# Performance work log

Measured on AMD Instinct MI355X. Metric: run time of the kernel, lower is better.

The kernel has to match this reference:

```python
import jax, jax.numpy as jnp
import numpy as np

B, L, D, H = 2, 2048, 768, 12
HD = D // H  # 64
BASE = 10000


def rope_tables(seq_len, head_dim, base):
    # inverse frequencies over even indices, angles [L, hd/2] -> duplicated to [L, hd]
    inv_freq = 1.0 / (base ** (jnp.arange(0, head_dim, 2, dtype=jnp.float32) / head_dim))
    angles = jnp.arange(seq_len, dtype=jnp.float32)[:, None] * inv_freq[None, :]
    cos = jnp.concatenate([jnp.cos(angles), jnp.cos(angles)], axis=-1)  # [L, hd]
    sin = jnp.concatenate([jnp.sin(angles), jnp.sin(angles)], axis=-1)
    return cos, sin


def rotate_half(x):
    x1, x2 = jnp.split(x, 2, axis=-1)
    return jnp.concatenate([-x2, x1], axis=-1)


def setup_inputs() -> dict:
    key = jax.random.key(0)
    k0, k1, k2 = jax.random.split(key, 3)
    s = 0.02
    return {
        "input_embeddings": jax.random.normal(k0, (B, L, D), dtype=jnp.float32),
        "w_qkv": jax.random.normal(k1, (D, 3 * D), dtype=jnp.float32) * s,
        "b_qkv": jnp.zeros((3 * D,), dtype=jnp.float32),
        "w_out": jax.random.normal(k2, (D, D), dtype=jnp.float32) * s,
        "b_out": jnp.zeros((D,), dtype=jnp.float32),
    }


def reference(input_embeddings, w_qkv, b_qkv, w_out, b_out):
    # QKV projection and head split: b l (h d) -> b h l d
    qkv = input_embeddings @ w_qkv + b_qkv
    q, k, v = jnp.split(qkv, 3, axis=-1)
    to_heads = lambda t: t.reshape(B, L, H, HD).transpose(0, 2, 1, 3)
    q, k, v = map(to_heads, (q, k, v))

    # RoPE (start_pos=0, no kv cache)
    cos, sin = rope_tables(L, HD, BASE)  # [L, HD], broadcasts over b,h
    q = q * cos + rotate_half(q) * sin
    k = k * cos + rotate_half(k) * sin

    # NOTE: source divides by sqrt(d.size(3)) = sqrt(key_seq_len), not sqrt(head_dim)
    scores = jnp.einsum("bhqd,bhkd->bhqk", q, k) / jnp.sqrt(jnp.float32(L))

    causal_mask = jnp.triu(jnp.ones((L, L), dtype=bool), 1)
    neg_inf = -jnp.finfo(scores.dtype).max
    scores = jnp.where(causal_mask, neg_inf, scores)

    probs = jax.nn.softmax(scores, axis=-1)  # dropout disabled (eval)
    attn_out = jnp.einsum("bhqk,bhkd->bhqd", probs, v)
    attn_out = attn_out.transpose(0, 2, 1, 3).reshape(B, L, D)  # b h l d -> b l (h d)
    output = attn_out @ w_out + b_out
    return output, probs
```

## Files before the change

kernel.cpp:

```cpp
#include <hip/hip_runtime.h>
#include <math.h>

#define B_  2
#define L_  2048
#define D_  768
#define H_  12
#define HD_ 64
#define M_  (B_*L_)
#define N3_ (3*D_)
#define OUT_ELEMS ((size_t)B_*L_*D_)

static constexpr float kScale = 0.022097086912079608f;
static constexpr float kLog2_10000_div32 = 0.415241011860920f;

typedef __attribute__((ext_vector_type(8))) short short8;
typedef __attribute__((ext_vector_type(4))) float f32x4;

__device__ __forceinline__ unsigned short f2bf(float f) {
  union { float f; unsigned u; } v; v.f = f;
  unsigned r = v.u + 0x7FFFu + ((v.u >> 16) & 1u);
  return (unsigned short)(r >> 16);
}

__device__ __forceinline__ void async_cp16(const void* g, void* l) {
  __builtin_amdgcn_global_load_lds((const __attribute__((address_space(1))) void*)g,
                                   (__attribute__((address_space(3))) void*)l, 16, 0, 0);
}

__global__ __launch_bounds__(256) void bf16conv_kernel(const float* __restrict__ in,
                                                       unsigned short* __restrict__ out)
{
  const int idx = blockIdx.x * 256 + threadIdx.x;
  const float* src = in + (size_t)idx * 8;
  float4 a = *(const float4*)src;
  float4 b = *(const float4*)(src + 4);
  unsigned short t[8];
  t[0] = f2bf(a.x); t[1] = f2bf(a.y); t[2] = f2bf(a.z); t[3] = f2bf(a.w);
  t[4] = f2bf(b.x); t[5] = f2bf(b.y); t[6] = f2bf(b.z); t[7] = f2bf(b.w);
  *(uint4*)(out + (size_t)idx * 8) = *(uint4*)t;
}

__global__ __launch_bounds__(256) void wtrans_kernel(const float* __restrict__ in,
                                                     unsigned short* __restrict__ out,
                                                     int K, int N)
{
  __shared__ __align__(16) unsigned short T[64][72];
  const int n0 = blockIdx.x * 64;
  const int k0 = blockIdx.y * 64;
  const int tid = threadIdx.x;
  const int row = tid >> 2;
  const int col = (tid & 3) * 16;
  {
    const float* src = in + (size_t)(k0 + row) * N + n0 + col;
    unsigned short tmp[16];
#pragma unroll
    for (int j = 0; j < 16; j += 4) {
      float4 v = *(const float4*)(src + j);
      tmp[j] = f2bf(v.x); tmp[j + 1] = f2bf(v.y); tmp[j + 2] = f2bf(v.z); tmp[j + 3] = f2bf(v.w);
    }
    *(uint4*)&T[row][col]     = *(uint4*)tmp;
    *(uint4*)&T[row][col + 8] = *(uint4*)(tmp + 8);
  }
  __syncthreads();
  unsigned short tmp[16];
#pragma unroll
  for (int j = 0; j < 16; ++j) tmp[j] = T[col + j][row];
  unsigned short* dst = out + (size_t)(n0 + row) * K + k0 + col;
  *(uint4*)dst       = *(uint4*)tmp;
  *(uint4*)(dst + 8) = *(uint4*)(tmp + 8);
}

__global__ __launch_bounds__(256) void vtrans_kernel(const unsigned short* __restrict__ vb,
                                                     unsigned short* __restrict__ vt)
{
  __shared__ __align__(16) unsigned short T[64][72];
  const int bh = blockIdx.y;
  const int l0 = blockIdx.x * 64;
  const int tid = threadIdx.x;
  const int row = tid >> 2;
  const int col = (tid & 3) * 16;
  {
    const unsigned short* src = vb + ((size_t)bh * L_ + l0 + row) * HD_ + col;
    *(uint4*)&T[row][col]     = *(const uint4*)src;
    *(uint4*)&T[row][col + 8] = *(const uint4*)(src + 8);
  }
  __syncthreads();
  unsigned short tmp[16];
#pragma unroll
  for (int j = 0; j < 16; ++j) tmp[j] = T[col + j][row];
  unsigned short* dst = vt + ((size_t)bh * HD_ + row) * L_ + l0 + col;
  *(uint4*)dst       = *(uint4*)tmp;
  *(uint4*)(dst + 8) = *(uint4*)(tmp + 8);
}

__global__ __launch_bounds__(256) void gemm_mfma_kernel(
    const unsigned short* __restrict__ A, const unsigned short* __restrict__ Bt,
    const float* __restrict__ bias, float* __restrict__ C,
    int M, int N, int K, int mode,
    unsigned short* __restrict__ qp, unsigned short* __restrict__ kp,
    unsigned short* __restrict__ vp)
{
  __shared__ __align__(16) unsigned short As[128 * 32];
  __shared__ __align__(16) unsigned short Bs[128 * 32];

  const int tid  = threadIdx.x;
  const int w    = tid >> 6;
  const int lane = tid & 63;
  const int m16  = lane & 15;
  const int quad = lane >> 4;
  const int wr   = w & 1;
  const int wc   = w >> 1;

  const int bm = blockIdx.y * 128;
  const int bn = blockIdx.x * 128;

  const int s0 = w * 128 + lane;
  const int s1 = s0 + 64;
  const int r0 = s0 >> 2, c0 = (s0 & 3) ^ (r0 & 3);
  const int r1 = s1 >> 2, c1 = (s1 & 3) ^ (r1 & 3);
  const unsigned short* gA0 = A + (size_t)(bm + r0) * K + c0 * 8;
  const unsigned short* gA1 = A + (size_t)(bm + r1) * K + c1 * 8;
  const unsigned short* gB0 = Bt + (size_t)(bn + r0) * K + c0 * 8;
  const unsigned short* gB1 = Bt + (size_t)(bn + r1) * K + c1 * 8;
  unsigned short* lA0 = As + (w * 128) * 8;
  unsigned short* lA1 = As + (w * 128 + 64) * 8;
  unsigned short* lB0 = Bs + (w * 128) * 8;
  unsigned short* lB1 = Bs + (w * 128 + 64) * 8;

  const int sw = quad ^ (m16 & 3);
  const short8* pA[4];
  const short8* pB[4];
#pragma unroll
  for (int i = 0; i < 4; ++i) {
    const int ra = wr * 64 + i * 16 + m16;
    const int rb = wc * 64 + i * 16 + m16;
    pA[i] = (const short8*)(As + ra * 32 + sw * 8);
    pB[i] = (const short8*)(Bs + rb * 32 + sw * 8);
  }

  f32x4 acc[4][4];
#pragma unroll
  for (int i = 0; i < 4; ++i)
#pragma unroll
    for (int j = 0; j < 4; ++j) { acc[i][j][0] = 0.f; acc[i][j][1] = 0.f; acc[i][j][2] = 0.f; acc[i][j][3] = 0.f; }

  for (int k0 = 0; k0 < K; k0 += 32) {
    async_cp16(gA0 + k0, lA0);
    async_cp16(gA1 + k0, lA1);
    async_cp16(gB0 + k0, lB0);
    async_cp16(gB1 + k0, lB1);
    __syncthreads();
    short8 af[4], bfr[4];
#pragma unroll
    for (int i = 0; i < 4; ++i) { af[i] = *pA[i]; bfr[i] = *pB[i]; }
#pragma unroll
    for (int i = 0; i < 4; ++i)
#pragma unroll
      for (int j = 0; j < 4; ++j)
        acc[i][j] = __builtin_amdgcn_mfma_f32_16x16x32_bf16(af[i], bfr[j], acc[i][j], 0, 0, 0);
    __syncthreads();
  }

  if (mode == 0) {
#pragma unroll
    for (int j = 0; j < 4; ++j) {
      const int n = bn + wc * 64 + j * 16 + m16;
      const float bj = bias[n];
#pragma unroll
      for (int i = 0; i < 4; ++i) {
        const int mrow = bm + wr * 64 + i * 16 + quad * 4;
#pragma unroll
        for (int r2 = 0; r2 < 4; ++r2)
          C[(size_t)(mrow + r2) * N + n] = acc[i][j][r2] + bj;
      }
    }
  } else {
    const int segbase = bn + wc * 64;
    const int which = segbase / D_;
    const int h = (segbase - which * D_) >> 6;
    unsigned short* dstT = (which == 0) ? qp : (which == 1) ? kp : vp;
    float bj[4];
#pragma unroll
    for (int og = 0; og < 4; ++og) bj[og] = bias[segbase + og * 16 + m16];
    const float invfA = exp2f(-(float)m16 * kLog2_10000_div32);
    const float invfB = exp2f(-(float)(16 + m16) * kLog2_10000_div32);

#pragma unroll
    for (int i = 0; i < 4; ++i) {
      const int mrow = bm + wr * 64 + i * 16 + quad * 4;
#pragma unroll
      for (int r2 = 0; r2 < 4; ++r2) {
        const int m = mrow + r2;
        const int bi = m >> 11;
        const int li = m & (L_ - 1);
        float vals[4];
#pragma unroll
        for (int og = 0; og < 4; ++og) vals[og] = acc[i][og][r2] + bj[og];
        unsigned short* drow = dstT + (((size_t)(bi * H_ + h)) * L_ + li) * HD_;
        if (which == 2) {
#pragma unroll
          for (int og = 0; og < 4; ++og) drow[og * 16 + m16] = f2bf(vals[og]);
        } else {
          const float fl = (float)li;
#pragma unroll
          for (int og = 0; og < 4; ++og) {
            const int d = og * 16 + m16;
            const float theta = fl * ((og & 1) ? invfB : invfA);
            float sv, cv;
            __sincosf(theta, &sv, &cv);
            const float part = vals[og ^ 2];
            const float rot = (og < 2) ? -part : part;
            drow[d] = f2bf(vals[og] * cv + rot * sv);
          }
        }
      }
    }
  }
}

__global__ __launch_bounds__(256) void attn_mfma_kernel(
    const unsigned short* __restrict__ qb, const unsigned short* __restrict__ kb,
    const unsigned short* __restrict__ vt, float* __restrict__ probs,
    unsigned short* __restrict__ attnb)
{
  __shared__ __align__(16) unsigned short Ks[64][72];
  __shared__ __align__(16) unsigned short Vs[64][72];
  __shared__ __align__(16) unsigned short Pb[4][16][72];

  const int tid  = threadIdx.x;
  const int w    = tid >> 6;
  const int lane = tid & 63;
  const int m16  = lane & 15;
  const int quad = lane >> 4;

  const int bh = blockIdx.y;
  const int qt = (int)gridDim.x - 1 - (int)blockIdx.x;
  const int q0 = qt * 64;
  const int bb = bh / H_;
  const int hh = bh - bb * H_;
  const int ktiles = qt + 1;
  const int qrow_base = q0 + w * 16;

  const unsigned short* kbase = kb + (size_t)bh * L_ * HD_;
  const unsigned short* vbase = vt + (size_t)bh * HD_ * L_;

  const unsigned short* qp = qb + ((size_t)bh * L_ + qrow_base + m16) * HD_ + quad * 8;
  const short8 qf0 = *(const short8*)(qp);
  const short8 qf1 = *(const short8*)(qp + 32);

  const int srow = tid >> 2;
  const int scol = (tid & 3) * 16;

  float lsum[4] = {0.f, 0.f, 0.f, 0.f};
  for (int kt = 0; kt < ktiles; ++kt) {
    const int k0 = kt * 64;
    __syncthreads();
    {
      const unsigned short* src = kbase + (size_t)(k0 + srow) * HD_ + scol;
      *(uint4*)&Ks[srow][scol]     = *(const uint4*)src;
      *(uint4*)&Ks[srow][scol + 8] = *(const uint4*)(src + 8);
    }
    __syncthreads();
#pragma unroll
    for (int cg = 0; cg < 4; ++cg) {
      const short8 b0 = *(const short8*)&Ks[cg * 16 + m16][quad * 8];
      const short8 b1 = *(const short8*)&Ks[cg * 16 + m16][32 + quad * 8];
      f32x4 s = {0.f, 0.f, 0.f, 0.f};
      s = __builtin_amdgcn_mfma_f32_16x16x32_bf16(qf0, b0, s, 0, 0, 0);
      s = __builtin_amdgcn_mfma_f32_16x16x32_bf16(qf1, b1, s, 0, 0, 0);
      const int kcol = k0 + cg * 16 + m16;
#pragma unroll
      for (int r2 = 0; r2 < 4; ++r2) {
        const int qrow = qrow_base + quad * 4 + r2;
        const float e = __expf(s[r2] * kScale);
        lsum[r2] += (kcol <= qrow) ? e : 0.f;
      }
    }
  }
  float linv[4];
#pragma unroll
  for (int r2 = 0; r2 < 4; ++r2) {
    float v = lsum[r2];
    v += __shfl_xor(v, 1, 64);
    v += __shfl_xor(v, 2, 64);
    v += __shfl_xor(v, 4, 64);
    v += __shfl_xor(v, 8, 64);
    linv[r2] = 1.f / v;
  }

  f32x4 oacc[4];
#pragma unroll
  for (int og = 0; og < 4; ++og) { oacc[og][0]=0.f; oacc[og][1]=0.f; oacc[og][2]=0.f; oacc[og][3]=0.f; }

  for (int kt = 0; kt < ktiles; ++kt) {
    const int k0 = kt * 64;
    __syncthreads();
    {
      const unsigned short* srck = kbase + (size_t)(k0 + srow) * HD_ + scol;
      *(uint4*)&Ks[srow][scol]     = *(const uint4*)srck;
      *(uint4*)&Ks[srow][scol + 8] = *(const uint4*)(srck + 8);
      const unsigned short* srcv = vbase + (size_t)srow * L_ + k0 + scol;
      *(uint4*)&Vs[srow][scol]     = *(const uint4*)srcv;
      *(uint4*)&Vs[srow][scol + 8] = *(const uint4*)(srcv + 8);
    }
    __syncthreads();
#pragma unroll
    for (int cg = 0; cg < 4; ++cg) {
      const short8 b0 = *(const short8*)&Ks[cg * 16 + m16][quad * 8];
      const short8 b1 = *(const short8*)&Ks[cg * 16 + m16][32 + quad * 8];
      f32x4 s = {0.f, 0.f, 0.f, 0.f};
      s = __builtin_amdgcn_mfma_f32_16x16x32_bf16(qf0, b0, s, 0, 0, 0);
      s = __builtin_amdgcn_mfma_f32_16x16x32_bf16(qf1, b1, s, 0, 0, 0);
      const int kcol = k0 + cg * 16 + m16;
#pragma unroll
      for (int r2 = 0; r2 < 4; ++r2) {
        const int qrow = qrow_base + quad * 4 + r2;
        const float p = (kcol <= qrow) ? __expf(s[r2] * kScale) * linv[r2] : 0.f;
        probs[((size_t)bh * L_ + qrow) * L_ + kcol] = p;
        Pb[w][quad * 4 + r2][cg * 16 + m16] = f2bf(p);
      }
    }
    const short8 pa0 = *(const short8*)&Pb[w][m16][quad * 8];
    const short8 pa1 = *(const short8*)&Pb[w][m16][32 + quad * 8];
#pragma unroll
    for (int og = 0; og < 4; ++og) {
      const short8 v0 = *(const short8*)&Vs[og * 16 + m16][quad * 8];
      const short8 v1 = *(const short8*)&Vs[og * 16 + m16][32 + quad * 8];
      oacc[og] = __builtin_amdgcn_mfma_f32_16x16x32_bf16(pa0, v0, oacc[og], 0, 0, 0);
      oacc[og] = __builtin_amdgcn_mfma_f32_16x16x32_bf16(pa1, v1, oacc[og], 0, 0, 0);
    }
  }

  {
    const float4 z4 = make_float4(0.f, 0.f, 0.f, 0.f);
#pragma unroll
    for (int r2 = 0; r2 < 4; ++r2) {
      float* pr = probs + ((size_t)bh * L_ + qrow_base + quad * 4 + r2) * L_;
      for (int c0 = ktiles * 64; c0 < L_; c0 += 64)
        *(float4*)(pr + c0 + m16 * 4) = z4;
    }
  }

#pragma unroll
  for (int og = 0; og < 4; ++og)
#pragma unroll
    for (int r2 = 0; r2 < 4; ++r2)
      attnb[((size_t)bb * L_ + qrow_base + quad * 4 + r2) * D_ + hh * HD_ + og * 16 + m16] =
          f2bf(oacc[og][r2]);
}

extern "C" void kernel_launch(void* const* d_in, const int* in_sizes, int n_in,
                              void* d_out, int out_size, void* d_ws, size_t ws_size,
                              hipStream_t stream)
{
  const float* x     = (const float*)d_in[0];
  const float* w_qkv = (const float*)d_in[1];
  const float* b_qkv = (const float*)d_in[2];
  const float* w_out = (const float*)d_in[3];
  const float* b_out = (const float*)d_in[4];

  float* out   = (float*)d_out;
  float* probs = out + OUT_ELEMS;

  const size_t NE = (size_t)B_ * H_ * L_ * HD_;
  unsigned short* qbw   = (unsigned short*)d_ws;
  unsigned short* kbw   = qbw + NE;
  unsigned short* vbw   = kbw + NE;
  unsigned short* vtw   = vbw + NE;
  unsigned short* xbw   = vtw + NE;
  unsigned short* attnb = xbw + NE;
  unsigned short* wqT   = attnb + NE;
  unsigned short* woT   = wqT + (size_t)N3_ * D_;

  bf16conv_kernel<<<(int)(OUT_ELEMS / 8 / 256), 256, 0, stream>>>(x, xbw);
  wtrans_kernel<<<dim3(N3_ / 64, D_ / 64), 256, 0, stream>>>(w_qkv, wqT, D_, N3_);
  wtrans_kernel<<<dim3(D_ / 64, D_ / 64), 256, 0, stream>>>(w_out, woT, D_, D_);

  gemm_mfma_kernel<<<dim3(N3_ / 128, M_ / 128), 256, 0, stream>>>(
      xbw, wqT, b_qkv, nullptr, M_, N3_, D_, 1, qbw, kbw, vbw);

  vtrans_kernel<<<dim3(L_ / 64, B_ * H_), 256, 0, stream>>>(vbw, vtw);

  attn_mfma_kernel<<<dim3(L_ / 64, B_ * H_), 256, 0, stream>>>(qbw, kbw, vtw, probs, attnb);

  gemm_mfma_kernel<<<dim3(D_ / 128, M_ / 128), 256, 0, stream>>>(
      attnb, woT, b_out, out, M_, D_, D_, 0, nullptr, nullptr, nullptr);
}
```

Before: 565.9 us.

## Drop block barriers in attention: direct K fragment loads, per-wave V staging with prefetch

Removes the shared K tile and both __syncthreads per key tile. Each wave now loads its K MFMA fragments straight from global memory and stages V into its own private LDS slice, with the next tile's V prefetched into registers. Probability and zero-fill stores become nontemporal, and the attention output write moves ahead of the zero-fill. Waves no longer wait on each other, but each wave now issues roughly four times the global K/V traffic that the old shared tile loads did, and register pressure goes up.

```diff
diff --git a/kernel.cpp b/kernel.cpp
--- a/kernel.cpp
+++ b/kernel.cpp
@@ -223,8 +223,7 @@
     const unsigned short* __restrict__ vt, float* __restrict__ probs,
     unsigned short* __restrict__ attnb)
 {
-  __shared__ __align__(16) unsigned short Ks[64][72];
-  __shared__ __align__(16) unsigned short Vs[64][72];
+  __shared__ __align__(16) unsigned short Vs[4][64][72];
   __shared__ __align__(16) unsigned short Pb[4][16][72];
 
   const int tid  = threadIdx.x;
@@ -248,26 +247,23 @@
   const short8 qf0 = *(const short8*)(qp);
   const short8 qf1 = *(const short8*)(qp + 32);
 
-  const int srow = tid >> 2;
-  const int scol = (tid & 3) * 16;
+  const unsigned short* kfp = kbase + (size_t)m16 * HD_ + quad * 8;
 
   float lsum[4] = {0.f, 0.f, 0.f, 0.f};
   for (int kt = 0; kt < ktiles; ++kt) {
     const int k0 = kt * 64;
-    __syncthreads();
-    {
-      const unsigned short* src = kbase + (size_t)(k0 + srow) * HD_ + scol;
-      *(uint4*)&Ks[srow][scol]     = *(const uint4*)src;
-      *(uint4*)&Ks[srow][scol + 8] = *(const uint4*)(src + 8);
-    }
-    __syncthreads();
+    short8 kb0[4], kb1[4];
 #pragma unroll
     for (int cg = 0; cg < 4; ++cg) {
-      const short8 b0 = *(const short8*)&Ks[cg * 16 + m16][quad * 8];
-      const short8 b1 = *(const short8*)&Ks[cg * 16 + m16][32 + quad * 8];
+      const unsigned short* kr = kfp + (size_t)(k0 + cg * 16) * HD_;
+      kb0[cg] = *(const short8*)(kr);
+      kb1[cg] = *(const short8*)(kr + 32);
+    }
+#pragma unroll
+    for (int cg = 0; cg < 4; ++cg) {
       f32x4 s = {0.f, 0.f, 0.f, 0.f};
-      s = __builtin_amdgcn_mfma_f32_16x16x32_bf16(qf0, b0, s, 0, 0, 0);
-      s = __builtin_amdgcn_mfma_f32_16x16x32_bf16(qf1, b1, s, 0, 0, 0);
+      s = __builtin_amdgcn_mfma_f32_16x16x32_bf16(qf0, kb0[cg], s, 0, 0, 0);
+      s = __builtin_amdgcn_mfma_f32_16x16x32_bf16(qf1, kb1[cg], s, 0, 0, 0);
       const int kcol = k0 + cg * 16 + m16;
 #pragma unroll
       for (int r2 = 0; r2 < 4; ++r2) {
@@ -292,31 +288,52 @@
 #pragma unroll
   for (int og = 0; og < 4; ++og) { oacc[og][0]=0.f; oacc[og][1]=0.f; oacc[og][2]=0.f; oacc[og][3]=0.f; }
 
+  unsigned short* Vw = &Vs[w][0][0];
+  const int vr = lane >> 2;
+  const int vc = (lane & 3) * 16;
+  const unsigned short* vsrc0 = vbase + (size_t)vr * L_ + vc;
+
+  uint4 vstg[8];
+#pragma unroll
+  for (int j = 0; j < 4; ++j) {
+    const unsigned short* s = vsrc0 + (size_t)(16 * j) * L_;
+    vstg[2 * j]     = *(const uint4*)s;
+    vstg[2 * j + 1] = *(const uint4*)(s + 8);
+  }
+
   for (int kt = 0; kt < ktiles; ++kt) {
     const int k0 = kt * 64;
-    __syncthreads();
-    {
-      const unsigned short* srck = kbase + (size_t)(k0 + srow) * HD_ + scol;
-      *(uint4*)&Ks[srow][scol]     = *(const uint4*)srck;
-      *(uint4*)&Ks[srow][scol + 8] = *(const uint4*)(srck + 8);
-      const unsigned short* srcv = vbase + (size_t)srow * L_ + k0 + scol;
-      *(uint4*)&Vs[srow][scol]     = *(const uint4*)srcv;
-      *(uint4*)&Vs[srow][scol + 8] = *(const uint4*)(srcv + 8);
-    }
-    __syncthreads();
+#pragma unroll
+    for (int j = 0; j < 4; ++j) {
+      unsigned short* d = Vw + (vr + 16 * j) * 72 + vc;
+      *(uint4*)d       = vstg[2 * j];
+      *(uint4*)(d + 8) = vstg[2 * j + 1];
+    }
+    short8 kb0[4], kb1[4];
 #pragma unroll
     for (int cg = 0; cg < 4; ++cg) {
-      const short8 b0 = *(const short8*)&Ks[cg * 16 + m16][quad * 8];
-      const short8 b1 = *(const short8*)&Ks[cg * 16 + m16][32 + quad * 8];
+      const unsigned short* kr = kfp + (size_t)(k0 + cg * 16) * HD_;
+      kb0[cg] = *(const short8*)(kr);
+      kb1[cg] = *(const short8*)(kr + 32);
+    }
+    const int k0n = (kt + 1 < ktiles) ? k0 + 64 : k0;
+#pragma unroll
+    for (int j = 0; j < 4; ++j) {
+      const unsigned short* s = vsrc0 + (size_t)(16 * j) * L_ + k0n;
+      vstg[2 * j]     = *(const uint4*)s;
+      vstg[2 * j + 1] = *(const uint4*)(s + 8);
+    }
+#pragma unroll
+    for (int cg = 0; cg < 4; ++cg) {
       f32x4 s = {0.f, 0.f, 0.f, 0.f};
-      s = __builtin_amdgcn_mfma_f32_16x16x32_bf16(qf0, b0, s, 0, 0, 0);
-      s = __builtin_amdgcn_mfma_f32_16x16x32_bf16(qf1, b1, s, 0, 0, 0);
+      s = __builtin_amdgcn_mfma_f32_16x16x32_bf16(qf0, kb0[cg], s, 0, 0, 0);
+      s = __builtin_amdgcn_mfma_f32_16x16x32_bf16(qf1, kb1[cg], s, 0, 0, 0);
       const int kcol = k0 + cg * 16 + m16;
 #pragma unroll
       for (int r2 = 0; r2 < 4; ++r2) {
         const int qrow = qrow_base + quad * 4 + r2;
         const float p = (kcol <= qrow) ? __expf(s[r2] * kScale) * linv[r2] : 0.f;
-        probs[((size_t)bh * L_ + qrow) * L_ + kcol] = p;
+        __builtin_nontemporal_store(p, &probs[((size_t)bh * L_ + qrow) * L_ + kcol]);
         Pb[w][quad * 4 + r2][cg * 16 + m16] = f2bf(p);
       }
     }
@@ -324,29 +341,29 @@
     const short8 pa1 = *(const short8*)&Pb[w][m16][32 + quad * 8];
 #pragma unroll
     for (int og = 0; og < 4; ++og) {
-      const short8 v0 = *(const short8*)&Vs[og * 16 + m16][quad * 8];
-      const short8 v1 = *(const short8*)&Vs[og * 16 + m16][32 + quad * 8];
+      const short8 v0 = *(const short8*)(Vw + (og * 16 + m16) * 72 + quad * 8);
+      const short8 v1 = *(const short8*)(Vw + (og * 16 + m16) * 72 + 32 + quad * 8);
       oacc[og] = __builtin_amdgcn_mfma_f32_16x16x32_bf16(pa0, v0, oacc[og], 0, 0, 0);
       oacc[og] = __builtin_amdgcn_mfma_f32_16x16x32_bf16(pa1, v1, oacc[og], 0, 0, 0);
     }
   }
 
+#pragma unroll
+  for (int og = 0; og < 4; ++og)
+#pragma unroll
+    for (int r2 = 0; r2 < 4; ++r2)
+      attnb[((size_t)bb * L_ + qrow_base + quad * 4 + r2) * D_ + hh * HD_ + og * 16 + m16] =
+          f2bf(oacc[og][r2]);
+
   {
-    const float4 z4 = make_float4(0.f, 0.f, 0.f, 0.f);
+    const f32x4 z4 = {0.f, 0.f, 0.f, 0.f};
 #pragma unroll
     for (int r2 = 0; r2 < 4; ++r2) {
       float* pr = probs + ((size_t)bh * L_ + qrow_base + quad * 4 + r2) * L_;
       for (int c0 = ktiles * 64; c0 < L_; c0 += 64)
-        *(float4*)(pr + c0 + m16 * 4) = z4;
-    }
-  }
-
-#pragma unroll
-  for (int og = 0; og < 4; ++og)
-#pragma unroll
-    for (int r2 = 0; r2 < 4; ++r2)
-      attnb[((size_t)bb * L_ + qrow_base + quad * 4 + r2) * D_ + hh * HD_ + og * 16 + m16] =
-          f2bf(oacc[og][r2]);
+        __builtin_nontemporal_store(z4, (f32x4*)(pr + c0 + m16 * 4));
+    }
+  }
 }
 
 extern "C" void kernel_launch(void* const* d_in, const int* in_sizes, int n_in,
```

Measured after the change: 788.3 us. 39.3% more time.
